# Kernel tuning notes

Hardware: AMD Instinct MI355X
Metric: run time of the kernel (lower is better)

The kernel has to match this reference:

```python
import jax, jax.numpy as jnp
import numpy as np

B = 16
N_IN_PER = 256
N_SKIP_PER = 1024
C_IN = 256
C_SKIP = 128


def setup_inputs() -> dict:
    key = jax.random.key(0)
    ks = jax.random.split(key, 8)
    n_in = B * N_IN_PER
    n_skip = B * N_SKIP_PER
    in_x = jax.random.normal(ks[0], (n_in, C_IN), dtype=jnp.float32)
    in_pos = jax.random.uniform(ks[1], (n_in, 3), dtype=jnp.float32)
    in_batch = jnp.repeat(jnp.arange(B, dtype=jnp.int64), N_IN_PER)
    skip_x = jax.random.normal(ks[2], (n_skip, C_SKIP), dtype=jnp.float32)
    skip_pos = jax.random.uniform(ks[3], (n_skip, 3), dtype=jnp.float32)
    skip_batch = jnp.repeat(jnp.arange(B, dtype=jnp.int64), N_SKIP_PER)
    d_cat = C_IN + C_SKIP + 3  # 387
    W1 = jax.random.normal(ks[4], (d_cat, 256), dtype=jnp.float32) * (1.0 / np.sqrt(d_cat))
    b1 = jnp.zeros((256,), dtype=jnp.float32)
    W2 = jax.random.normal(ks[5], (256, 256), dtype=jnp.float32) * (1.0 / 16.0)
    b2 = jnp.zeros((256,), dtype=jnp.float32)
    return {"in_x": in_x, "in_pos": in_pos, "in_batch": in_batch,
            "skip_x": skip_x, "skip_pos": skip_pos, "skip_batch": skip_batch,
            "W1": W1, "b1": b1, "W2": W2, "b2": b2, "knn_num": 3}


def _knn_interpolate(in_x, in_pos, in_batch, skip_pos, skip_batch, k):
    # Pairwise squared distances fine->coarse, masked across graphs. [Ns, Ni]
    d2 = jnp.sum((skip_pos[:, None, :] - in_pos[None, :, :]) ** 2, axis=-1)
    cross = skip_batch[:, None] != in_batch[None, :]
    d2 = jnp.where(cross, jnp.inf, d2)
    _, idx = jax.lax.top_k(-d2, k)  # [Ns, k] nearest coarse neighbors
    nb_pos = in_pos[idx]  # [Ns, k, 3]
    dist = jnp.sqrt(jnp.sum((nb_pos - skip_pos[:, None, :]) ** 2, axis=-1))
    dist = jnp.maximum(dist, 1e-10)
    w = 1.0 / dist
    w = w / (jnp.sum(w, axis=-1, keepdims=True) + 1e-16)  # per-target normalization
    return jnp.einsum('nk,nkc->nc', w, in_x[idx])  # [Ns, C_in]


def reference(in_x, in_pos, in_batch, skip_x, skip_pos, skip_batch, W1, b1, W2, b2, knn_num):
    interp = _knn_interpolate(in_x, in_pos, in_batch, skip_pos, skip_batch, knn_num)
    h = jnp.concatenate([interp, skip_x, skip_pos], axis=1)  # [Ns, 387]
    h = jax.nn.relu(h @ W1 + b1)
    h = jax.nn.relu(h @ W2 + b2)
    return h
```

## Files before the change

kernel.cpp:

```cpp
#include <hip/hip_runtime.h>
#include <hip/hip_bf16.h>


typedef __bf16 bf16x8 __attribute__((ext_vector_type(8)));
typedef float  f32x4  __attribute__((ext_vector_type(4)));

__device__ __forceinline__ unsigned short f2bf(float f) {
  __hip_bfloat16 h = __float2bfloat16(f);
  return __builtin_bit_cast(unsigned short, h);
}

#define GLDS16(G, L)                                                          \
  __builtin_amdgcn_global_load_lds(                                           \
      (const __attribute__((address_space(1))) void*)(G),                     \
      (__attribute__((address_space(3))) void*)(L), 16, 0, 0)

#define BAR()    __builtin_amdgcn_s_barrier()
#define WAITV(N) asm volatile("s_waitcnt vmcnt(" #N ")" ::: "memory")
#define WAITL()  asm volatile("s_waitcnt lgkmcnt(0)" ::: "memory")

static constexpr int MROWS = 16384;
static constexpr int KPAD  = 416;
static constexpr int KREAL = 387;
static constexpr int NK1   = 13;
static constexpr int NK2   = 8;
static constexpr int H1STR = 264;

__global__ __launch_bounds__(256) void knn_prep(
    const float* __restrict__ in_x,
    const float* __restrict__ in_pos,
    const float* __restrict__ skip_x,
    const float* __restrict__ skip_pos,
    const float* __restrict__ W1, const float* __restrict__ W2,
    unsigned short* __restrict__ W1t, unsigned short* __restrict__ W2t,
    unsigned short* __restrict__ H)
{
  __shared__ float T[64][65];
  __shared__ float P[3][256];
  const int tid = threadIdx.x;

  if (blockIdx.x < 44) {
    int b = blockIdx.x;
    const float* S; unsigned short* D; int KP, Kreal, kb, nb;
    if (b < 28) { S = W1; D = W1t; KP = KPAD; Kreal = KREAL; kb = b >> 2; nb = b & 3; }
    else { b -= 28; S = W2; D = W2t; KP = 256; Kreal = 256; kb = b >> 2; nb = b & 3; }
    const int k0 = kb << 6, n0 = nb << 6;
    const int tr = tid >> 4, tc = tid & 15;
#pragma unroll
    for (int i = 0; i < 4; ++i) {
      const int k = k0 + i * 16 + tr;
      float4 v = make_float4(0.f, 0.f, 0.f, 0.f);
      if (k < Kreal) v = *(const float4*)(S + (size_t)k * 256 + n0 + tc * 4);
      T[i * 16 + tr][tc * 4 + 0] = v.x;
      T[i * 16 + tr][tc * 4 + 1] = v.y;
      T[i * 16 + tr][tc * 4 + 2] = v.z;
      T[i * 16 + tr][tc * 4 + 3] = v.w;
    }
    __syncthreads();
#pragma unroll
    for (int i = 0; i < 4; ++i) {
      const int n = n0 + i * 16 + tr;
      const int k = k0 + tc * 4;
      if (k < KP) {
        ushort4 o;
        o.x = f2bf(T[tc * 4 + 0][i * 16 + tr]);
        o.y = f2bf(T[tc * 4 + 1][i * 16 + tr]);
        o.z = f2bf(T[tc * 4 + 2][i * 16 + tr]);
        o.w = f2bf(T[tc * 4 + 3][i * 16 + tr]);
        *(ushort4*)(D + (size_t)n * KP + k) = o;
      }
    }
    return;
  }

  const int s0 = (blockIdx.x - 44) << 2;
  const int ib = (s0 >> 10) << 8;
  {
    const float* bp = in_pos + (size_t)ib * 3;
    for (int i = tid; i < 768; i += 256) P[i % 3][i / 3] = bp[i];
  }
  __syncthreads();

  const int wid = tid >> 6, lane = tid & 63;
  const int s = s0 + wid;
  const float sx = skip_pos[(size_t)s * 3 + 0];
  const float sy = skip_pos[(size_t)s * 3 + 1];
  const float sz = skip_pos[(size_t)s * 3 + 2];

  float d2[4];
#pragma unroll
  for (int q = 0; q < 4; ++q) {
    const int i = lane + (q << 6);
    const float dx = __fsub_rn(sx, P[0][i]);
    const float dy = __fsub_rn(sy, P[1][i]);
    const float dz = __fsub_rn(sz, P[2][i]);
    d2[q] = __fadd_rn(__fadd_rn(__fmul_rn(dx, dx), __fmul_rn(dy, dy)),
                      __fmul_rn(dz, dz));
  }

  int gsel[3]; float wsel[3]; float wsum = 0.f;
#pragma unroll
  for (int p = 0; p < 3; ++p) {
    float bd = d2[0]; int bi = lane;
#pragma unroll
    for (int q = 1; q < 4; ++q) {
      const int i = lane + (q << 6);
      if (d2[q] < bd) { bd = d2[q]; bi = i; }
    }
#pragma unroll
    for (int m = 1; m < 64; m <<= 1) {
      const float od = __shfl_xor(bd, m);
      const int   oi = __shfl_xor(bi, m);
      if (od < bd || (od == bd && oi < bi)) { bd = od; bi = oi; }
    }
    const bool win = ((bi & 63) == lane);
    const int  qw  = bi >> 6;
    d2[0] = (win && qw == 0) ? 3.4e38f : d2[0];
    d2[1] = (win && qw == 1) ? 3.4e38f : d2[1];
    d2[2] = (win && qw == 2) ? 3.4e38f : d2[2];
    d2[3] = (win && qw == 3) ? 3.4e38f : d2[3];
    gsel[p] = bi;
    const float w = 1.0f / fmaxf(sqrtf(bd), 1e-10f);
    wsel[p] = w; wsum += w;
  }
  const float denom = wsum + 1e-16f;
  const float w0 = wsel[0] / denom;
  const float w1 = wsel[1] / denom;
  const float w2 = wsel[2] / denom;

  const f32x4 a = *(const f32x4*)(in_x + (size_t)(ib + gsel[0]) * 256 + lane * 4);
  const f32x4 b = *(const f32x4*)(in_x + (size_t)(ib + gsel[1]) * 256 + lane * 4);
  const f32x4 c = *(const f32x4*)(in_x + (size_t)(ib + gsel[2]) * 256 + lane * 4);

  unsigned short* hr = H + (size_t)s * KPAD;
  ushort4 o4;
  o4.x = f2bf(w0 * a.x + w1 * b.x + w2 * c.x);
  o4.y = f2bf(w0 * a.y + w1 * b.y + w2 * c.y);
  o4.z = f2bf(w0 * a.z + w1 * b.z + w2 * c.z);
  o4.w = f2bf(w0 * a.w + w1 * b.w + w2 * c.w);
  *(ushort4*)(hr + (lane << 2)) = o4;

  const float2 sv = ((const float2*)(skip_x + (size_t)s * 128))[lane];
  ushort2 o2; o2.x = f2bf(sv.x); o2.y = f2bf(sv.y);
  *(ushort2*)(hr + 256 + (lane << 1)) = o2;

  if (lane < 32) {
    float v = (lane == 0) ? sx : (lane == 1) ? sy : (lane == 2) ? sz : 0.f;
    hr[384 + lane] = f2bf(v);
  }
}

__global__ __launch_bounds__(256) void gemm12(
    const unsigned short* __restrict__ Hg,
    const unsigned short* __restrict__ W1t,
    const unsigned short* __restrict__ W2t,
    const float* __restrict__ bias1, const float* __restrict__ bias2,
    float* __restrict__ out)
{
  __shared__ unsigned short As[4][64 * 32];
  __shared__ unsigned short Bs[4][256 * 32];
  __shared__ unsigned short h1s[64 * H1STR];

  const int tid = threadIdx.x, lane = tid & 63, wid = tid >> 6;
  const int m0 = blockIdx.x << 6;
  const int fr = lane & 15, g = lane >> 4;
  const int wcc = wid << 6;

  const int r  = tid >> 2;
  const int cs = (tid & 3) ^ ((r >> 1) & 3);
  const unsigned short* gA   = Hg  + (size_t)(m0 + r) * KPAD + cs * 8;
  const unsigned short* gB10 = W1t + (size_t)r * KPAD + cs * 8;
  const unsigned short* gB20 = W2t + (size_t)r * 256  + cs * 8;

#define STAGE1(ks, bu)                                                        \
  {                                                                           \
    const int _ko = (ks) * 32;                                                \
    GLDS16(gA + _ko, &As[bu][wid * 512]);                                     \
    GLDS16(gB10 + _ko,                 &Bs[bu][wid * 512]);                   \
    GLDS16(gB10 + 64 * KPAD + _ko,     &Bs[bu][2048 + wid * 512]);            \
    GLDS16(gB10 + 128 * KPAD + _ko,    &Bs[bu][4096 + wid * 512]);            \
    GLDS16(gB10 + 192 * KPAD + _ko,    &Bs[bu][6144 + wid * 512]);            \
  }
#define STAGE2(ks, bu)                                                        \
  {                                                                           \
    const int _ko = (ks) * 32;                                                \
    GLDS16(gB20 + _ko,                 &Bs[bu][wid * 512]);                   \
    GLDS16(gB20 + 64 * 256 + _ko,      &Bs[bu][2048 + wid * 512]);            \
    GLDS16(gB20 + 128 * 256 + _ko,     &Bs[bu][4096 + wid * 512]);            \
    GLDS16(gB20 + 192 * 256 + _ko,     &Bs[bu][6144 + wid * 512]);            \
  }

  STAGE1(0, 0); STAGE1(1, 1); STAGE1(2, 2);

  int woff[4], hoff[4], h2off[4];
#pragma unroll
  for (int i = 0; i < 4; ++i) {
    const int Rw = wcc + i * 16 + fr;
    const int Rh = i * 16 + fr;
    woff[i]  = Rw * 32 + ((g ^ ((Rw >> 1) & 3)) << 3);
    hoff[i]  = Rh * 32 + ((g ^ ((Rh >> 1) & 3)) << 3);
    h2off[i] = Rh * H1STR + g * 8;
  }

  f32x4 bv1[4], bv2[4];
#pragma unroll
  for (int mc = 0; mc < 4; ++mc) {
    bv1[mc] = *(const f32x4*)(bias1 + wcc + mc * 16 + g * 4);
    bv2[mc] = *(const f32x4*)(bias2 + wcc + mc * 16 + g * 4);
  }

  f32x4 acc[4][4] = {};

#pragma unroll 1
  for (int ks = 0; ks < NK1; ++ks) {
    if (ks + 3 < NK1) STAGE1(ks + 3, (ks + 3) & 3);
    const int rem = NK1 - 1 - ks;
    if (rem >= 3)      { WAITV(15); }
    else if (rem == 2) { WAITV(10); }
    else if (rem == 1) { WAITV(5); }
    else               { WAITV(0); }
    BAR();
    const unsigned short* as = As[ks & 3];
    const unsigned short* bs = Bs[ks & 3];
    bf16x8 wf[4], hf[4];
#pragma unroll
    for (int i = 0; i < 4; ++i) wf[i] = *(const bf16x8*)&bs[woff[i]];
#pragma unroll
    for (int i = 0; i < 4; ++i) hf[i] = *(const bf16x8*)&as[hoff[i]];
#pragma unroll
    for (int mc = 0; mc < 4; ++mc)
#pragma unroll
      for (int rr = 0; rr < 4; ++rr)
        acc[mc][rr] = __builtin_amdgcn_mfma_f32_16x16x32_bf16(
            wf[mc], hf[rr], acc[mc][rr], 0, 0, 0);
    WAITL(); BAR();
  }

  STAGE2(0, 0); STAGE2(1, 1); STAGE2(2, 2);

#pragma unroll
  for (int rr = 0; rr < 4; ++rr)
#pragma unroll
    for (int mc = 0; mc < 4; ++mc) {
      ushort4 o;
      o.x = f2bf(fmaxf(acc[mc][rr][0] + bv1[mc][0], 0.f));
      o.y = f2bf(fmaxf(acc[mc][rr][1] + bv1[mc][1], 0.f));
      o.z = f2bf(fmaxf(acc[mc][rr][2] + bv1[mc][2], 0.f));
      o.w = f2bf(fmaxf(acc[mc][rr][3] + bv1[mc][3], 0.f));
      *(ushort4*)&h1s[(rr * 16 + fr) * H1STR + wcc + mc * 16 + g * 4] = o;
    }
  WAITL(); BAR();

#pragma unroll
  for (int mc = 0; mc < 4; ++mc)
#pragma unroll
    for (int rr = 0; rr < 4; ++rr) acc[mc][rr] = f32x4{0.f, 0.f, 0.f, 0.f};

#pragma unroll 1
  for (int ks = 0; ks < NK2; ++ks) {
    if (ks + 3 < NK2) STAGE2(ks + 3, (ks + 3) & 3);
    const int rem = NK2 - 1 - ks;
    if (rem >= 3)      { WAITV(12); }
    else if (rem == 2) { WAITV(8); }
    else if (rem == 1) { WAITV(4); }
    else               { WAITV(0); }
    BAR();
    const unsigned short* bs = Bs[ks & 3];
    bf16x8 wf[4], hf[4];
#pragma unroll
    for (int i = 0; i < 4; ++i) wf[i] = *(const bf16x8*)&bs[woff[i]];
#pragma unroll
    for (int i = 0; i < 4; ++i) hf[i] = *(const bf16x8*)&h1s[h2off[i] + ks * 32];
#pragma unroll
    for (int mc = 0; mc < 4; ++mc)
#pragma unroll
      for (int rr = 0; rr < 4; ++rr)
        acc[mc][rr] = __builtin_amdgcn_mfma_f32_16x16x32_bf16(
            wf[mc], hf[rr], acc[mc][rr], 0, 0, 0);
    WAITL(); BAR();
  }
#undef STAGE1
#undef STAGE2

#pragma unroll
  for (int rr = 0; rr < 4; ++rr) {
    const size_t row = (size_t)(m0 + rr * 16 + fr);
#pragma unroll
    for (int mc = 0; mc < 4; ++mc) {
      f32x4 o;
#pragma unroll
      for (int j = 0; j < 4; ++j) o[j] = fmaxf(acc[mc][rr][j] + bv2[mc][j], 0.f);
      *(f32x4*)(out + row * 256 + wcc + mc * 16 + g * 4) = o;
    }
  }
}

extern "C" void kernel_launch(void* const* d_in, const int* in_sizes, int n_in,
                              void* d_out, int out_size, void* d_ws, size_t ws_size,
                              hipStream_t stream) {
  const float* in_x     = (const float*)d_in[0];
  const float* in_pos   = (const float*)d_in[1];
  const float* skip_x   = (const float*)d_in[3];
  const float* skip_pos = (const float*)d_in[4];
  const float* W1       = (const float*)d_in[6];
  const float* bias1    = (const float*)d_in[7];
  const float* W2       = (const float*)d_in[8];
  const float* bias2    = (const float*)d_in[9];

  char* ws = (char*)d_ws;
  unsigned short* W1t = (unsigned short*)(ws);
  unsigned short* W2t = (unsigned short*)(ws + 212992);
  unsigned short* H   = (unsigned short*)(ws + 212992 + 131072);

  knn_prep<<<dim3(44 + MROWS / 4), dim3(256), 0, stream>>>(
      in_x, in_pos, skip_x, skip_pos, W1, W2, W1t, W2t, H);
  gemm12<<<dim3(MROWS / 64), dim3(256), 0, stream>>>(
      H, W1t, W2t, bias1, bias2, (float*)d_out);
}
```

Measured before the change: 40.28 us.

## Replace LDS-staged pipelined GEMM with direct global fragment loads, 8 waves

```diff
diff --git a/kernel.cpp b/kernel.cpp
--- a/kernel.cpp
+++ b/kernel.cpp
@@ -10,20 +10,11 @@
   return __builtin_bit_cast(unsigned short, h);
 }
 
-#define GLDS16(G, L)                                                          \
-  __builtin_amdgcn_global_load_lds(                                           \
-      (const __attribute__((address_space(1))) void*)(G),                     \
-      (__attribute__((address_space(3))) void*)(L), 16, 0, 0)
-
-#define BAR()    __builtin_amdgcn_s_barrier()
-#define WAITV(N) asm volatile("s_waitcnt vmcnt(" #N ")" ::: "memory")
-#define WAITL()  asm volatile("s_waitcnt lgkmcnt(0)" ::: "memory")
-
 static constexpr int MROWS = 16384;
-static constexpr int KPAD  = 416;
+static constexpr int KP1   = 448;
 static constexpr int KREAL = 387;
-static constexpr int NK1   = 13;
-static constexpr int NK2   = 8;
+static constexpr int NK1   = 7;
+static constexpr int NK2   = 4;
 static constexpr int H1STR = 264;
 
 __global__ __launch_bounds__(256) void knn_prep(
@@ -42,7 +33,7 @@
   if (blockIdx.x < 44) {
     int b = blockIdx.x;
     const float* S; unsigned short* D; int KP, Kreal, kb, nb;
-    if (b < 28) { S = W1; D = W1t; KP = KPAD; Kreal = KREAL; kb = b >> 2; nb = b & 3; }
+    if (b < 28) { S = W1; D = W1t; KP = KP1; Kreal = KREAL; kb = b >> 2; nb = b & 3; }
     else { b -= 28; S = W2; D = W2t; KP = 256; Kreal = 256; kb = b >> 2; nb = b & 3; }
     const int k0 = kb << 6, n0 = nb << 6;
     const int tr = tid >> 4, tc = tid & 15;
@@ -132,7 +123,7 @@
   const f32x4 b = *(const f32x4*)(in_x + (size_t)(ib + gsel[1]) * 256 + lane * 4);
   const f32x4 c = *(const f32x4*)(in_x + (size_t)(ib + gsel[2]) * 256 + lane * 4);
 
-  unsigned short* hr = H + (size_t)s * KPAD;
+  unsigned short* hr = H + (size_t)s * KP1;
   ushort4 o4;
   o4.x = f2bf(w0 * a.x + w1 * b.x + w2 * c.x);
   o4.y = f2bf(w0 * a.y + w1 * b.y + w2 * c.y);
@@ -144,153 +135,124 @@
   ushort2 o2; o2.x = f2bf(sv.x); o2.y = f2bf(sv.y);
   *(ushort2*)(hr + 256 + (lane << 1)) = o2;
 
-  if (lane < 32) {
-    float v = (lane == 0) ? sx : (lane == 1) ? sy : (lane == 2) ? sz : 0.f;
+  {
+    const float v = (lane == 0) ? sx : (lane == 1) ? sy : (lane == 2) ? sz : 0.f;
     hr[384 + lane] = f2bf(v);
   }
 }
 
-__global__ __launch_bounds__(256) void gemm12(
+__global__ __launch_bounds__(512) void gemm12b(
     const unsigned short* __restrict__ Hg,
     const unsigned short* __restrict__ W1t,
     const unsigned short* __restrict__ W2t,
     const float* __restrict__ bias1, const float* __restrict__ bias2,
     float* __restrict__ out)
 {
-  __shared__ unsigned short As[4][64 * 32];
-  __shared__ unsigned short Bs[4][256 * 32];
   __shared__ unsigned short h1s[64 * H1STR];
 
   const int tid = threadIdx.x, lane = tid & 63, wid = tid >> 6;
   const int m0 = blockIdx.x << 6;
   const int fr = lane & 15, g = lane >> 4;
-  const int wcc = wid << 6;
-
-  const int r  = tid >> 2;
-  const int cs = (tid & 3) ^ ((r >> 1) & 3);
-  const unsigned short* gA   = Hg  + (size_t)(m0 + r) * KPAD + cs * 8;
-  const unsigned short* gB10 = W1t + (size_t)r * KPAD + cs * 8;
-  const unsigned short* gB20 = W2t + (size_t)r * 256  + cs * 8;
-
-#define STAGE1(ks, bu)                                                        \
-  {                                                                           \
-    const int _ko = (ks) * 32;                                                \
-    GLDS16(gA + _ko, &As[bu][wid * 512]);                                     \
-    GLDS16(gB10 + _ko,                 &Bs[bu][wid * 512]);                   \
-    GLDS16(gB10 + 64 * KPAD + _ko,     &Bs[bu][2048 + wid * 512]);            \
-    GLDS16(gB10 + 128 * KPAD + _ko,    &Bs[bu][4096 + wid * 512]);            \
-    GLDS16(gB10 + 192 * KPAD + _ko,    &Bs[bu][6144 + wid * 512]);            \
-  }
-#define STAGE2(ks, bu)                                                        \
-  {                                                                           \
-    const int _ko = (ks) * 32;                                                \
-    GLDS16(gB20 + _ko,                 &Bs[bu][wid * 512]);                   \
-    GLDS16(gB20 + 64 * 256 + _ko,      &Bs[bu][2048 + wid * 512]);            \
-    GLDS16(gB20 + 128 * 256 + _ko,     &Bs[bu][4096 + wid * 512]);            \
-    GLDS16(gB20 + 192 * 256 + _ko,     &Bs[bu][6144 + wid * 512]);            \
-  }
-
-  STAGE1(0, 0); STAGE1(1, 1); STAGE1(2, 2);
-
-  int woff[4], hoff[4], h2off[4];
-#pragma unroll
-  for (int i = 0; i < 4; ++i) {
-    const int Rw = wcc + i * 16 + fr;
-    const int Rh = i * 16 + fr;
-    woff[i]  = Rw * 32 + ((g ^ ((Rw >> 1) & 3)) << 3);
-    hoff[i]  = Rh * 32 + ((g ^ ((Rh >> 1) & 3)) << 3);
-    h2off[i] = Rh * H1STR + g * 8;
-  }
-
-  f32x4 bv1[4], bv2[4];
-#pragma unroll
-  for (int mc = 0; mc < 4; ++mc) {
-    bv1[mc] = *(const f32x4*)(bias1 + wcc + mc * 16 + g * 4);
-    bv2[mc] = *(const f32x4*)(bias2 + wcc + mc * 16 + g * 4);
-  }
-
-  f32x4 acc[4][4] = {};
-
-#pragma unroll 1
+  const int c0 = wid << 5;
+
+  const unsigned short* ph[4];
+  const unsigned short* pw[2];
+#pragma unroll
+  for (int j = 0; j < 4; ++j)
+    ph[j] = Hg + (size_t)(m0 + j * 16 + fr) * KP1 + g * 8;
+#pragma unroll
+  for (int i = 0; i < 2; ++i)
+    pw[i] = W1t + (size_t)(c0 + i * 16 + fr) * KP1 + g * 8;
+
+  f32x4 acc[2][4] = {};
+
+#pragma unroll
   for (int ks = 0; ks < NK1; ++ks) {
-    if (ks + 3 < NK1) STAGE1(ks + 3, (ks + 3) & 3);
-    const int rem = NK1 - 1 - ks;
-    if (rem >= 3)      { WAITV(15); }
-    else if (rem == 2) { WAITV(10); }
-    else if (rem == 1) { WAITV(5); }
-    else               { WAITV(0); }
-    BAR();
-    const unsigned short* as = As[ks & 3];
-    const unsigned short* bs = Bs[ks & 3];
-    bf16x8 wf[4], hf[4];
-#pragma unroll
-    for (int i = 0; i < 4; ++i) wf[i] = *(const bf16x8*)&bs[woff[i]];
-#pragma unroll
-    for (int i = 0; i < 4; ++i) hf[i] = *(const bf16x8*)&as[hoff[i]];
-#pragma unroll
-    for (int mc = 0; mc < 4; ++mc)
-#pragma unroll
-      for (int rr = 0; rr < 4; ++rr)
-        acc[mc][rr] = __builtin_amdgcn_mfma_f32_16x16x32_bf16(
-            wf[mc], hf[rr], acc[mc][rr], 0, 0, 0);
-    WAITL(); BAR();
-  }
-
-  STAGE2(0, 0); STAGE2(1, 1); STAGE2(2, 2);
-
-#pragma unroll
-  for (int rr = 0; rr < 4; ++rr)
-#pragma unroll
-    for (int mc = 0; mc < 4; ++mc) {
+    bf16x8 wf[2][2], hf[4][2];
+#pragma unroll
+    for (int kk = 0; kk < 2; ++kk) {
+#pragma unroll
+      for (int i = 0; i < 2; ++i)
+        wf[i][kk] = *(const bf16x8*)(pw[i] + ks * 64 + kk * 32);
+#pragma unroll
+      for (int j = 0; j < 4; ++j)
+        hf[j][kk] = *(const bf16x8*)(ph[j] + ks * 64 + kk * 32);
+    }
+#pragma unroll
+    for (int kk = 0; kk < 2; ++kk)
+#pragma unroll
+      for (int mc = 0; mc < 2; ++mc)
+#pragma unroll
+        for (int rf = 0; rf < 4; ++rf)
+          acc[mc][rf] = __builtin_amdgcn_mfma_f32_16x16x32_bf16(
+              wf[mc][kk], hf[rf][kk], acc[mc][rf], 0, 0, 0);
+  }
+
+  f32x4 bv1[2];
+#pragma unroll
+  for (int mc = 0; mc < 2; ++mc)
+    bv1[mc] = *(const f32x4*)(bias1 + c0 + mc * 16 + g * 4);
+#pragma unroll
+  for (int rf = 0; rf < 4; ++rf)
+#pragma unroll
+    for (int mc = 0; mc < 2; ++mc) {
       ushort4 o;
-      o.x = f2bf(fmaxf(acc[mc][rr][0] + bv1[mc][0], 0.f));
-      o.y = f2bf(fmaxf(acc[mc][rr][1] + bv1[mc][1], 0.f));
-      o.z = f2bf(fmaxf(acc[mc][rr][2] + bv1[mc][2], 0.f));
-      o.w = f2bf(fmaxf(acc[mc][rr][3] + bv1[mc][3], 0.f));
-      *(ushort4*)&h1s[(rr * 16 + fr) * H1STR + wcc + mc * 16 + g * 4] = o;
-    }
-  WAITL(); BAR();
-
-#pragma unroll
-  for (int mc = 0; mc < 4; ++mc)
-#pragma unroll
-    for (int rr = 0; rr < 4; ++rr) acc[mc][rr] = f32x4{0.f, 0.f, 0.f, 0.f};
-
-#pragma unroll 1
+      o.x = f2bf(fmaxf(acc[mc][rf][0] + bv1[mc][0], 0.f));
+      o.y = f2bf(fmaxf(acc[mc][rf][1] + bv1[mc][1], 0.f));
+      o.z = f2bf(fmaxf(acc[mc][rf][2] + bv1[mc][2], 0.f));
+      o.w = f2bf(fmaxf(acc[mc][rf][3] + bv1[mc][3], 0.f));
+      *(ushort4*)&h1s[(rf * 16 + fr) * H1STR + c0 + mc * 16 + g * 4] = o;
+    }
+  __syncthreads();
+
+#pragma unroll
+  for (int mc = 0; mc < 2; ++mc)
+#pragma unroll
+    for (int rf = 0; rf < 4; ++rf) acc[mc][rf] = f32x4{0.f, 0.f, 0.f, 0.f};
+
+  const unsigned short* pw2[2];
+#pragma unroll
+  for (int i = 0; i < 2; ++i)
+    pw2[i] = W2t + (size_t)(c0 + i * 16 + fr) * 256 + g * 8;
+  const int hbase[4] = {
+      (0 * 16 + fr) * H1STR + g * 8, (1 * 16 + fr) * H1STR + g * 8,
+      (2 * 16 + fr) * H1STR + g * 8, (3 * 16 + fr) * H1STR + g * 8};
+
+#pragma unroll
   for (int ks = 0; ks < NK2; ++ks) {
-    if (ks + 3 < NK2) STAGE2(ks + 3, (ks + 3) & 3);
-    const int rem = NK2 - 1 - ks;
-    if (rem >= 3)      { WAITV(12); }
-    else if (rem == 2) { WAITV(8); }
-    else if (rem == 1) { WAITV(4); }
-    else               { WAITV(0); }
-    BAR();
-    const unsigned short* bs = Bs[ks & 3];
-    bf16x8 wf[4], hf[4];
-#pragma unroll
-    for (int i = 0; i < 4; ++i) wf[i] = *(const bf16x8*)&bs[woff[i]];
-#pragma unroll
-    for (int i = 0; i < 4; ++i) hf[i] = *(const bf16x8*)&h1s[h2off[i] + ks * 32];
-#pragma unroll
-    for (int mc = 0; mc < 4; ++mc)
-#pragma unroll
-      for (int rr = 0; rr < 4; ++rr)
-        acc[mc][rr] = __builtin_amdgcn_mfma_f32_16x16x32_bf16(
-            wf[mc], hf[rr], acc[mc][rr], 0, 0, 0);
-    WAITL(); BAR();
-  }
-#undef STAGE1
-#undef STAGE2
-
-#pragma unroll
-  for (int rr = 0; rr < 4; ++rr) {
-    const size_t row = (size_t)(m0 + rr * 16 + fr);
-#pragma unroll
-    for (int mc = 0; mc < 4; ++mc) {
+    bf16x8 wf[2][2], hf[4][2];
+#pragma unroll
+    for (int kk = 0; kk < 2; ++kk) {
+#pragma unroll
+      for (int i = 0; i < 2; ++i)
+        wf[i][kk] = *(const bf16x8*)(pw2[i] + ks * 64 + kk * 32);
+#pragma unroll
+      for (int j = 0; j < 4; ++j)
+        hf[j][kk] = *(const bf16x8*)&h1s[hbase[j] + ks * 64 + kk * 32];
+    }
+#pragma unroll
+    for (int kk = 0; kk < 2; ++kk)
+#pragma unroll
+      for (int mc = 0; mc < 2; ++mc)
+#pragma unroll
+        for (int rf = 0; rf < 4; ++rf)
+          acc[mc][rf] = __builtin_amdgcn_mfma_f32_16x16x32_bf16(
+              wf[mc][kk], hf[rf][kk], acc[mc][rf], 0, 0, 0);
+  }
+
+  f32x4 bv2[2];
+#pragma unroll
+  for (int mc = 0; mc < 2; ++mc)
+    bv2[mc] = *(const f32x4*)(bias2 + c0 + mc * 16 + g * 4);
+#pragma unroll
+  for (int rf = 0; rf < 4; ++rf) {
+    const size_t row = (size_t)(m0 + rf * 16 + fr);
+#pragma unroll
+    for (int mc = 0; mc < 2; ++mc) {
       f32x4 o;
 #pragma unroll
-      for (int j = 0; j < 4; ++j) o[j] = fmaxf(acc[mc][rr][j] + bv2[mc][j], 0.f);
-      *(f32x4*)(out + row * 256 + wcc + mc * 16 + g * 4) = o;
+      for (int j = 0; j < 4; ++j) o[j] = fmaxf(acc[mc][rf][j] + bv2[mc][j], 0.f);
+      *(f32x4*)(out + row * 256 + c0 + mc * 16 + g * 4) = o;
     }
   }
 }
@@ -309,11 +271,11 @@
 
   char* ws = (char*)d_ws;
   unsigned short* W1t = (unsigned short*)(ws);
-  unsigned short* W2t = (unsigned short*)(ws + 212992);
-  unsigned short* H   = (unsigned short*)(ws + 212992 + 131072);
+  unsigned short* W2t = (unsigned short*)(ws + 229376);
+  unsigned short* H   = (unsigned short*)(ws + 229376 + 131072);
 
   knn_prep<<<dim3(44 + MROWS / 4), dim3(256), 0, stream>>>(
       in_x, in_pos, skip_x, skip_pos, W1, W2, W1t, W2t, H);
-  gemm12<<<dim3(MROWS / 64), dim3(256), 0, stream>>>(
+  gemm12b<<<dim3(MROWS / 64), dim3(512), 0, stream>>>(
       H, W1t, W2t, bias1, bias2, (float*)d_out);
 }
```

After: 46.34 us. 15.1% more time.
